# Kernel tuning notes

Measured on AMD Instinct MI355X. Metric: run time of the kernel, lower is better.

Reference implementation:

```python
import jax, jax.numpy as jnp
import numpy as np

BATCH = 65536
IN_A = 256
IN_B = 256
OUT = 64


def setup_inputs() -> dict:
    key = jax.random.key(0)
    k1, k2, k3, k4 = jax.random.split(key, 4)
    xa = jax.random.normal(k1, (BATCH, IN_A), dtype=jnp.float32)
    xb = jax.random.normal(k2, (BATCH, IN_B), dtype=jnp.float32)
    wa = jax.random.normal(k3, (IN_A, OUT), dtype=jnp.float32) * 0.05
    wb = jax.random.normal(k4, (IN_B, OUT), dtype=jnp.float32) * 0.05
    return {"xa": xa, "xb": xb, "wa": wa, "wb": wb}


def reference(xa, xb, wa, wb):
    # Plaintext semantics of the SSHE cross secret-shared matmul:
    # [z|rank_b] = [xa|rank_a] @ <wa> + [xb|rank_b] @ <wb>
    return xa @ wa + xb @ wb
```

## Files before the change

kernel.cpp:

```cpp
#include <hip/hip_runtime.h>
#include <stdint.h>


#define WT_SHORTS (512 * 64)
#define WT_BYTES  (WT_SHORTS * 2)

typedef __bf16 bf16x8 __attribute__((ext_vector_type(8)));
typedef float  f32x4  __attribute__((ext_vector_type(4)));

__global__ void prep_wt_kernel(const float* __restrict__ wa,
                               const float* __restrict__ wb,
                               __bf16* __restrict__ wt) {
    int o2 = blockIdx.x * 256 + threadIdx.x;
    #pragma unroll
    for (int h = 0; h < 2; ++h) {
        int o    = o2 * 2 + h;
        int j    = o & 7;
        int lane = (o >> 3) & 63;
        int cb   = (o >> 9) & 3;
        int s    = o >> 11;
        int k    = s * 32 + (lane >> 4) * 8 + j;
        int col  = (lane & 15) + cb * 16;
        float v  = (k < 256) ? wa[k * 64 + col] : wb[(k - 256) * 64 + col];
        wt[o] = (__bf16)v;
    }
}

template <bool USE_WS>
__global__ __launch_bounds__(512, 4)
void agg_gemm_kernel(const float* __restrict__ xa,
                     const float* __restrict__ xb,
                     const float* __restrict__ wa,
                     const float* __restrict__ wb,
                     const __bf16* __restrict__ wt,
                     float* __restrict__ out) {
    __shared__ __align__(16) __bf16 wlds[WT_SHORTS];

    const int t    = threadIdx.x;
    const int lane = t & 63;
    const int wave = t >> 6;

    if (USE_WS) {
        const f32x4* g = (const f32x4*)wt;
        f32x4*       l = (f32x4*)&wlds[0];
        #pragma unroll
        for (int it = 0; it < 8; ++it)
            l[it * 512 + t] = g[it * 512 + t];
    } else {
        for (int i = 0; i < 64; ++i) {
            int o    = t * 64 + i;
            int j    = o & 7;
            int ln   = (o >> 3) & 63;
            int cb   = (o >> 9) & 3;
            int s    = o >> 11;
            int k    = s * 32 + (ln >> 4) * 8 + j;
            int col  = (ln & 15) + cb * 16;
            wlds[o] = (__bf16)((k < 256) ? wa[k * 64 + col] : wb[(k - 256) * 64 + col]);
        }
    }
    __syncthreads();

    const int gw   = blockIdx.x * 8 + wave;
    const int tile = gw * 16;
    const int row  = lane & 15;
    const int kg   = lane >> 4;

    const float* prow_a = xa + (size_t)(tile + row) * 256 + kg * 8;
    const float* prow_b = xb + (size_t)(tile + row) * 256 + kg * 8;

    f32x4 xr[4][2];
    #pragma unroll
    for (int s = 0; s < 4; ++s) {
        xr[s][0] = *(const f32x4*)(prow_a + s * 32);
        xr[s][1] = *(const f32x4*)(prow_a + s * 32 + 4);
    }

    f32x4 acc0 = {0.f, 0.f, 0.f, 0.f};
    f32x4 acc1 = acc0, acc2 = acc0, acc3 = acc0;

    #pragma unroll
    for (int s = 0; s < 16; ++s) {
        f32x4 x0 = xr[s & 3][0];
        f32x4 x1 = xr[s & 3][1];

        if (s < 12) {
            const int sp = s + 4;
            const float* p = (sp < 8) ? (prow_a + sp * 32)
                                      : (prow_b + (sp - 8) * 32);
            xr[s & 3][0] = *(const f32x4*)(p);
            xr[s & 3][1] = *(const f32x4*)(p + 4);
        }

        bf16x8 af;
        af[0] = (__bf16)x0[0]; af[1] = (__bf16)x0[1];
        af[2] = (__bf16)x0[2]; af[3] = (__bf16)x0[3];
        af[4] = (__bf16)x1[0]; af[5] = (__bf16)x1[1];
        af[6] = (__bf16)x1[2]; af[7] = (__bf16)x1[3];

        const __bf16* wb0 = &wlds[(s * 4 + 0) * 512 + lane * 8];
        bf16x8 w0 = *(const bf16x8*)(wb0);
        bf16x8 w1 = *(const bf16x8*)(wb0 + 512);
        bf16x8 w2 = *(const bf16x8*)(wb0 + 1024);
        bf16x8 w3 = *(const bf16x8*)(wb0 + 1536);

        acc0 = __builtin_amdgcn_mfma_f32_16x16x32_bf16(af, w0, acc0, 0, 0, 0);
        acc1 = __builtin_amdgcn_mfma_f32_16x16x32_bf16(af, w1, acc1, 0, 0, 0);
        acc2 = __builtin_amdgcn_mfma_f32_16x16x32_bf16(af, w2, acc2, 0, 0, 0);
        acc3 = __builtin_amdgcn_mfma_f32_16x16x32_bf16(af, w3, acc3, 0, 0, 0);
    }

    float* po = out + (size_t)(tile + kg * 4) * 64 + row;
    #pragma unroll
    for (int r = 0; r < 4; ++r) {
        po[r * 64 +  0] = acc0[r];
        po[r * 64 + 16] = acc1[r];
        po[r * 64 + 32] = acc2[r];
        po[r * 64 + 48] = acc3[r];
    }
}

extern "C" void kernel_launch(void* const* d_in, const int* in_sizes, int n_in,
                              void* d_out, int out_size, void* d_ws, size_t ws_size,
                              hipStream_t stream) {
    const float* xa = (const float*)d_in[0];
    const float* xb = (const float*)d_in[1];
    const float* wa = (const float*)d_in[2];
    const float* wb = (const float*)d_in[3];
    float* out = (float*)d_out;

    if (ws_size >= (size_t)WT_BYTES) {
        __bf16* wt = (__bf16*)d_ws;
        prep_wt_kernel<<<64, 256, 0, stream>>>(wa, wb, wt);
        agg_gemm_kernel<true><<<512, 512, 0, stream>>>(xa, xb, wa, wb, wt, out);
    } else {
        agg_gemm_kernel<false><<<512, 512, 0, stream>>>(xa, xb, wa, wb, nullptr, out);
    }
}
```

Measured before the change: 162.3 us.

## Stage X tiles through swizzled double-buffered LDS with coalesced row loads

Switches to 1024-thread blocks that each cover 256 rows. X panels are loaded with coalesced row-major f32x4 reads, converted to bf16, and written to a double-buffered, XOR-swizzled LDS panel, where MFMA reads its A fragments. Previously each lane read its own strided segments straight from global memory. This targets poor coalescing, at the cost of 64KB of extra LDS, a barrier per chunk, and lower occupancy. The initial barrier after the weight load is folded into the first panel barrier.

Result: no change. 162.7 us (+0.3%).

```diff
diff --git a/kernel.cpp b/kernel.cpp
--- a/kernel.cpp
+++ b/kernel.cpp
@@ -2,10 +2,12 @@
 #include <stdint.h>
 
 
-#define WT_SHORTS (512 * 64)
-#define WT_BYTES  (WT_SHORTS * 2)
+#define WT_SHORTS  (512 * 64)
+#define WT_BYTES   (WT_SHORTS * 2)
+#define XPAN_BYTES (256 * 64 * 2)
 
 typedef __bf16 bf16x8 __attribute__((ext_vector_type(8)));
+typedef __bf16 bf16x4 __attribute__((ext_vector_type(4)));
 typedef float  f32x4  __attribute__((ext_vector_type(4)));
 
 __global__ void prep_wt_kernel(const float* __restrict__ wa,
@@ -27,7 +29,7 @@
 }
 
 template <bool USE_WS>
-__global__ __launch_bounds__(512, 4)
+__global__ __launch_bounds__(1024, 4)
 void agg_gemm_kernel(const float* __restrict__ xa,
                      const float* __restrict__ xb,
                      const float* __restrict__ wa,
@@ -35,6 +37,7 @@
                      const __bf16* __restrict__ wt,
                      float* __restrict__ out) {
     __shared__ __align__(16) __bf16 wlds[WT_SHORTS];
+    __shared__ __align__(16) __bf16 xpan[2 * 256 * 64];
 
     const int t    = threadIdx.x;
     const int lane = t & 63;
@@ -44,72 +47,96 @@
         const f32x4* g = (const f32x4*)wt;
         f32x4*       l = (f32x4*)&wlds[0];
         #pragma unroll
-        for (int it = 0; it < 8; ++it)
-            l[it * 512 + t] = g[it * 512 + t];
+        for (int it = 0; it < 4; ++it)
+            l[it * 1024 + t] = g[it * 1024 + t];
     } else {
-        for (int i = 0; i < 64; ++i) {
-            int o    = t * 64 + i;
+        for (int i = 0; i < 32; ++i) {
+            int o    = t * 32 + i;
             int j    = o & 7;
             int ln   = (o >> 3) & 63;
             int cb   = (o >> 9) & 3;
             int s    = o >> 11;
             int k    = s * 32 + (ln >> 4) * 8 + j;
             int col  = (ln & 15) + cb * 16;
-            wlds[o] = (__bf16)((k < 256) ? wa[k * 64 + col] : wb[(k - 256) * 64 + col]);
+            wlds[o] = (__bf16)((k < 256) ? wa[k * 64 + col]
+                                         : wb[(k - 256) * 64 + col]);
         }
     }
-    __syncthreads();
 
-    const int gw   = blockIdx.x * 8 + wave;
-    const int tile = gw * 16;
-    const int row  = lane & 15;
-    const int kg   = lane >> 4;
+    const int row0 = blockIdx.x * 256;
 
-    const float* prow_a = xa + (size_t)(tile + row) * 256 + kg * 8;
-    const float* prow_b = xb + (size_t)(tile + row) * 256 + kg * 8;
+    const int srow = t >> 4;
+    const int sp   = t & 15;
 
-    f32x4 xr[4][2];
-    #pragma unroll
-    for (int s = 0; s < 4; ++s) {
-        xr[s][0] = *(const f32x4*)(prow_a + s * 32);
-        xr[s][1] = *(const f32x4*)(prow_a + s * 32 + 4);
-    }
+    auto issue = [&](int c, f32x4 (&r)[4]) {
+        const float* src = ((c < 4) ? xa : xb)
+                         + (size_t)row0 * 256 + (c & 3) * 64 + sp * 4;
+        #pragma unroll
+        for (int j = 0; j < 4; ++j)
+            r[j] = *(const f32x4*)(src + (size_t)(j * 64 + srow) * 256);
+    };
+
+    auto lds_write = [&](int c, const f32x4 (&r)[4]) {
+        char* buf = (char*)xpan + (c & 1) * XPAN_BYTES;
+        #pragma unroll
+        for (int j = 0; j < 4; ++j) {
+            int row = j * 64 + srow;
+            bf16x4 v;
+            v[0] = (__bf16)r[j][0]; v[1] = (__bf16)r[j][1];
+            v[2] = (__bf16)r[j][2]; v[3] = (__bf16)r[j][3];
+            *(bf16x4*)(buf + ((row * 128 + sp * 8) ^ ((row & 7) << 4))) = v;
+        }
+    };
+
+    const int r_     = lane & 15;
+    const int kg     = lane >> 4;
+    const int prow   = wave * 16 + r_;
+    const int xbyte0 = prow * 128 + kg * 16;
+    const int xsw    = (r_ & 7) << 4;
 
     f32x4 acc0 = {0.f, 0.f, 0.f, 0.f};
     f32x4 acc1 = acc0, acc2 = acc0, acc3 = acc0;
 
+    auto mstep = [&](int c) {
+        const char* buf = (const char*)xpan + (c & 1) * XPAN_BYTES;
+        #pragma unroll
+        for (int s = 0; s < 2; ++s) {
+            bf16x8 af = *(const bf16x8*)(buf + ((xbyte0 + s * 64) ^ xsw));
+            const int sg = c * 2 + s;
+            const __bf16* w0p = &wlds[(sg * 4) * 512 + lane * 8];
+            bf16x8 w0 = *(const bf16x8*)(w0p);
+            bf16x8 w1 = *(const bf16x8*)(w0p + 512);
+            bf16x8 w2 = *(const bf16x8*)(w0p + 1024);
+            bf16x8 w3 = *(const bf16x8*)(w0p + 1536);
+            acc0 = __builtin_amdgcn_mfma_f32_16x16x32_bf16(af, w0, acc0, 0, 0, 0);
+            acc1 = __builtin_amdgcn_mfma_f32_16x16x32_bf16(af, w1, acc1, 0, 0, 0);
+            acc2 = __builtin_amdgcn_mfma_f32_16x16x32_bf16(af, w2, acc2, 0, 0, 0);
+            acc3 = __builtin_amdgcn_mfma_f32_16x16x32_bf16(af, w3, acc3, 0, 0, 0);
+        }
+    };
+
+    f32x4 rA[4], rB[4];
+    issue(0, rA);
+    issue(1, rB);
+    lds_write(0, rA);
+    asm volatile("s_waitcnt lgkmcnt(0)" ::: "memory");
+    __builtin_amdgcn_s_barrier();
+
     #pragma unroll
-    for (int s = 0; s < 16; ++s) {
-        f32x4 x0 = xr[s & 3][0];
-        f32x4 x1 = xr[s & 3][1];
-
-        if (s < 12) {
-            const int sp = s + 4;
-            const float* p = (sp < 8) ? (prow_a + sp * 32)
-                                      : (prow_b + (sp - 8) * 32);
-            xr[s & 3][0] = *(const f32x4*)(p);
-            xr[s & 3][1] = *(const f32x4*)(p + 4);
+    for (int c = 0; c < 8; ++c) {
+        if (c < 6) {
+            if (c & 1) issue(c + 2, rB); else issue(c + 2, rA);
+            __builtin_amdgcn_sched_barrier(0);
         }
-
-        bf16x8 af;
-        af[0] = (__bf16)x0[0]; af[1] = (__bf16)x0[1];
-        af[2] = (__bf16)x0[2]; af[3] = (__bf16)x0[3];
-        af[4] = (__bf16)x1[0]; af[5] = (__bf16)x1[1];
-        af[6] = (__bf16)x1[2]; af[7] = (__bf16)x1[3];
-
-        const __bf16* wb0 = &wlds[(s * 4 + 0) * 512 + lane * 8];
-        bf16x8 w0 = *(const bf16x8*)(wb0);
-        bf16x8 w1 = *(const bf16x8*)(wb0 + 512);
-        bf16x8 w2 = *(const bf16x8*)(wb0 + 1024);
-        bf16x8 w3 = *(const bf16x8*)(wb0 + 1536);
-
-        acc0 = __builtin_amdgcn_mfma_f32_16x16x32_bf16(af, w0, acc0, 0, 0, 0);
-        acc1 = __builtin_amdgcn_mfma_f32_16x16x32_bf16(af, w1, acc1, 0, 0, 0);
-        acc2 = __builtin_amdgcn_mfma_f32_16x16x32_bf16(af, w2, acc2, 0, 0, 0);
-        acc3 = __builtin_amdgcn_mfma_f32_16x16x32_bf16(af, w3, acc3, 0, 0, 0);
+        if (c < 7) {
+            if (c & 1) lds_write(c + 1, rA); else lds_write(c + 1, rB);
+        }
+        mstep(c);
+        asm volatile("s_waitcnt lgkmcnt(0)" ::: "memory");
+        __builtin_amdgcn_s_barrier();
     }
 
-    float* po = out + (size_t)(tile + kg * 4) * 64 + row;
+    float* po = out + (size_t)(row0 + wave * 16 + kg * 4) * 64 + r_;
     #pragma unroll
     for (int r = 0; r < 4; ++r) {
         po[r * 64 +  0] = acc0[r];
@@ -131,8 +158,8 @@
     if (ws_size >= (size_t)WT_BYTES) {
         __bf16* wt = (__bf16*)d_ws;
         prep_wt_kernel<<<64, 256, 0, stream>>>(wa, wb, wt);
-        agg_gemm_kernel<true><<<512, 512, 0, stream>>>(xa, xb, wa, wb, wt, out);
+        agg_gemm_kernel<true><<<256, 1024, 0, stream>>>(xa, xb, wa, wb, wt, out);
     } else {
-        agg_gemm_kernel<false><<<512, 512, 0, stream>>>(xa, xb, wa, wb, nullptr, out);
+        agg_gemm_kernel<false><<<256, 1024, 0, stream>>>(xa, xb, wa, wb, nullptr, out);
     }
 }
```

## Stage X tiles through swizzled LDS with coalesced loads; read weights from global

Applied to the files above, without the earlier changes.

Rewrites the GEMM kernel so each wave loads its 16-row X tile with row-coalesced 16-byte loads, converts it to bf16 and writes it into a per-wave XOR-swizzled LDS buffer. MFMA A-fragments are then read from LDS, and the four 128-column chunks are double-buffered through registers with sched barriers. Weights are no longer staged in LDS; B-fragments come straight from the pre-swizzled global workspace, relying on L1/L2 caching. This drops the block-wide weight preload and __syncthreads, and fixes the strided per-lane X access pattern, at the cost of repeated global weight reads per wave.

Result: no change. 159.7 us (-1.6%).

```diff
diff --git a/kernel.cpp b/kernel.cpp
--- a/kernel.cpp
+++ b/kernel.cpp
@@ -6,6 +6,7 @@
 #define WT_BYTES  (WT_SHORTS * 2)
 
 typedef __bf16 bf16x8 __attribute__((ext_vector_type(8)));
+typedef __bf16 bf16x4 __attribute__((ext_vector_type(4)));
 typedef float  f32x4  __attribute__((ext_vector_type(4)));
 
 __global__ void prep_wt_kernel(const float* __restrict__ wa,
@@ -26,7 +27,7 @@
     }
 }
 
-template <bool USE_WS>
+template <bool DIRECT_W>
 __global__ __launch_bounds__(512, 4)
 void agg_gemm_kernel(const float* __restrict__ xa,
                      const float* __restrict__ xb,
@@ -34,88 +35,101 @@
                      const float* __restrict__ wb,
                      const __bf16* __restrict__ wt,
                      float* __restrict__ out) {
-    __shared__ __align__(16) __bf16 wlds[WT_SHORTS];
+    __shared__ __align__(16) __bf16 xlds[8 * 2048];
 
     const int t    = threadIdx.x;
     const int lane = t & 63;
     const int wave = t >> 6;
+    char* xbuf = (char*)&xlds[wave * 2048];
 
-    if (USE_WS) {
-        const f32x4* g = (const f32x4*)wt;
-        f32x4*       l = (f32x4*)&wlds[0];
+    const int    gw  = blockIdx.x * 8 + wave;
+    const size_t R   = (size_t)gw * 16;
+    const int    l5  = lane >> 5;
+    const int    l31 = lane & 31;
+    const int    col = lane & 15;
+    const int    kg  = lane >> 4;
+
+    auto issue = [&](int p, f32x4 (&r)[8]) {
+        const float* X    = (p < 2) ? xa : xb;
+        const float* base = X + R * 256 + (p & 1) * 128 + l31 * 4;
         #pragma unroll
-        for (int it = 0; it < 8; ++it)
-            l[it * 512 + t] = g[it * 512 + t];
-    } else {
-        for (int i = 0; i < 64; ++i) {
-            int o    = t * 64 + i;
-            int j    = o & 7;
-            int ln   = (o >> 3) & 63;
-            int cb   = (o >> 9) & 3;
-            int s    = o >> 11;
-            int k    = s * 32 + (ln >> 4) * 8 + j;
-            int col  = (ln & 15) + cb * 16;
-            wlds[o] = (__bf16)((k < 256) ? wa[k * 64 + col] : wb[(k - 256) * 64 + col]);
+        for (int i = 0; i < 8; ++i)
+            r[i] = *(const f32x4*)(base + (size_t)(2 * i + l5) * 256);
+    };
+
+    auto cvt_write = [&](const f32x4 (&r)[8]) {
+        #pragma unroll
+        for (int i = 0; i < 8; ++i) {
+            const int rl = 2 * i + l5;
+            bf16x4 v;
+            v[0] = (__bf16)r[i][0]; v[1] = (__bf16)r[i][1];
+            v[2] = (__bf16)r[i][2]; v[3] = (__bf16)r[i][3];
+            *(bf16x4*)(xbuf + rl * 256 + ((l31 * 8) ^ ((rl & 7) << 4))) = v;
         }
-    }
-    __syncthreads();
+    };
 
-    const int gw   = blockIdx.x * 8 + wave;
-    const int tile = gw * 16;
-    const int row  = lane & 15;
-    const int kg   = lane >> 4;
+    f32x4 acc[4];
+    #pragma unroll
+    for (int cb = 0; cb < 4; ++cb) acc[cb] = (f32x4){0.f, 0.f, 0.f, 0.f};
 
-    const float* prow_a = xa + (size_t)(tile + row) * 256 + kg * 8;
-    const float* prow_b = xb + (size_t)(tile + row) * 256 + kg * 8;
+    const int xsw = (col & 7) << 4;
 
-    f32x4 xr[4][2];
+    auto compute = [&](int p) {
+        #pragma unroll
+        for (int s = 0; s < 4; ++s) {
+            bf16x8 af = *(const bf16x8*)(xbuf + col * 256 +
+                                         ((s * 64 + kg * 16) ^ xsw));
+            const int sg = p * 4 + s;
+            bf16x8 wf[4];
+            if constexpr (!DIRECT_W) {
+                const __bf16* wp = wt + (size_t)(sg * 4) * 512 + lane * 8;
+                wf[0] = *(const bf16x8*)(wp);
+                wf[1] = *(const bf16x8*)(wp + 512);
+                wf[2] = *(const bf16x8*)(wp + 1024);
+                wf[3] = *(const bf16x8*)(wp + 1536);
+            } else {
+                const int k0 = sg * 32 + kg * 8;
+                const float* src = (sg < 8) ? wa : wb;
+                const int    kk  = (sg < 8) ? k0 : (k0 - 256);
+                #pragma unroll
+                for (int cb = 0; cb < 4; ++cb)
+                    #pragma unroll
+                    for (int j = 0; j < 8; ++j)
+                        wf[cb][j] = (__bf16)src[(kk + j) * 64 + col + cb * 16];
+            }
+            acc[0] = __builtin_amdgcn_mfma_f32_16x16x32_bf16(af, wf[0], acc[0], 0, 0, 0);
+            acc[1] = __builtin_amdgcn_mfma_f32_16x16x32_bf16(af, wf[1], acc[1], 0, 0, 0);
+            acc[2] = __builtin_amdgcn_mfma_f32_16x16x32_bf16(af, wf[2], acc[2], 0, 0, 0);
+            acc[3] = __builtin_amdgcn_mfma_f32_16x16x32_bf16(af, wf[3], acc[3], 0, 0, 0);
+        }
+    };
+
+    f32x4 rA[8], rB[8];
+    issue(0, rA);
+    issue(1, rB);
+    cvt_write(rA);
+    compute(0);
+
+    issue(2, rA);
+    __builtin_amdgcn_sched_barrier(0);
+    cvt_write(rB);
+    compute(1);
+
+    issue(3, rB);
+    __builtin_amdgcn_sched_barrier(0);
+    cvt_write(rA);
+    compute(2);
+
+    cvt_write(rB);
+    compute(3);
+
+    float* po = out + (R + kg * 4) * 64 + col;
     #pragma unroll
-    for (int s = 0; s < 4; ++s) {
-        xr[s][0] = *(const f32x4*)(prow_a + s * 32);
-        xr[s][1] = *(const f32x4*)(prow_a + s * 32 + 4);
-    }
-
-    f32x4 acc0 = {0.f, 0.f, 0.f, 0.f};
-    f32x4 acc1 = acc0, acc2 = acc0, acc3 = acc0;
-
-    #pragma unroll
-    for (int s = 0; s < 16; ++s) {
-        f32x4 x0 = xr[s & 3][0];
-        f32x4 x1 = xr[s & 3][1];
-
-        if (s < 12) {
-            const int sp = s + 4;
-            const float* p = (sp < 8) ? (prow_a + sp * 32)
-                                      : (prow_b + (sp - 8) * 32);
-            xr[s & 3][0] = *(const f32x4*)(p);
-            xr[s & 3][1] = *(const f32x4*)(p + 4);
-        }
-
-        bf16x8 af;
-        af[0] = (__bf16)x0[0]; af[1] = (__bf16)x0[1];
-        af[2] = (__bf16)x0[2]; af[3] = (__bf16)x0[3];
-        af[4] = (__bf16)x1[0]; af[5] = (__bf16)x1[1];
-        af[6] = (__bf16)x1[2]; af[7] = (__bf16)x1[3];
-
-        const __bf16* wb0 = &wlds[(s * 4 + 0) * 512 + lane * 8];
-        bf16x8 w0 = *(const bf16x8*)(wb0);
-        bf16x8 w1 = *(const bf16x8*)(wb0 + 512);
-        bf16x8 w2 = *(const bf16x8*)(wb0 + 1024);
-        bf16x8 w3 = *(const bf16x8*)(wb0 + 1536);
-
-        acc0 = __builtin_amdgcn_mfma_f32_16x16x32_bf16(af, w0, acc0, 0, 0, 0);
-        acc1 = __builtin_amdgcn_mfma_f32_16x16x32_bf16(af, w1, acc1, 0, 0, 0);
-        acc2 = __builtin_amdgcn_mfma_f32_16x16x32_bf16(af, w2, acc2, 0, 0, 0);
-        acc3 = __builtin_amdgcn_mfma_f32_16x16x32_bf16(af, w3, acc3, 0, 0, 0);
-    }
-
-    float* po = out + (size_t)(tile + kg * 4) * 64 + row;
-    #pragma unroll
-    for (int r = 0; r < 4; ++r) {
-        po[r * 64 +  0] = acc0[r];
-        po[r * 64 + 16] = acc1[r];
-        po[r * 64 + 32] = acc2[r];
-        po[r * 64 + 48] = acc3[r];
+    for (int rr = 0; rr < 4; ++rr) {
+        po[rr * 64 +  0] = acc[0][rr];
+        po[rr * 64 + 16] = acc[1][rr];
+        po[rr * 64 + 32] = acc[2][rr];
+        po[rr * 64 + 48] = acc[3][rr];
     }
 }
 
@@ -131,8 +145,8 @@
     if (ws_size >= (size_t)WT_BYTES) {
         __bf16* wt = (__bf16*)d_ws;
         prep_wt_kernel<<<64, 256, 0, stream>>>(wa, wb, wt);
-        agg_gemm_kernel<true><<<512, 512, 0, stream>>>(xa, xb, wa, wb, wt, out);
+        agg_gemm_kernel<false><<<512, 512, 0, stream>>>(xa, xb, wa, wb, wt, out);
     } else {
-        agg_gemm_kernel<false><<<512, 512, 0, stream>>>(xa, xb, wa, wb, nullptr, out);
+        agg_gemm_kernel<true><<<512, 512, 0, stream>>>(xa, xb, wa, wb, nullptr, out);
     }
 }
```
